# Optimization experiments

Hardware: AMD Instinct MI355X
Metric: run time of the kernel (lower is better)

## Reference

```python
import jax, jax.numpy as jnp
import numpy as np

B, H, W, C = 1, 64, 64, 256
HEADS, K, DIL = 8, 7, 2
HD = C // HEADS
FF = 4 * C
EPS = 1e-5
SCALE = 1.0 / float(np.sqrt(HD))


def _axis_indices(L, k, d):
    """NATTEN dilated neighborhood: per dilation-group clamped sliding window.
    Returns key indices [L,k] and relative-position-bias indices [L,k]."""
    i = np.arange(L)
    g, rem = i // d, i % d                      # position within dilation group
    lg = (L - rem + d - 1) // d                 # group length per position
    start = np.clip(g - k // 2, 0, lg - k)      # clamped window start (group coords)
    a = np.arange(k)
    kidx = (start[:, None] + a[None, :]) * d + rem[:, None]          # key coord
    bidx = start[:, None] + a[None, :] - g[:, None] + (k - 1)        # rpb coord in [0, 2k-2]
    return kidx.astype(np.int32), bidx.astype(np.int32)


def setup_inputs():
    key = jax.random.key(0)
    ks = jax.random.split(key, 8)
    p = lambda k_, sh: jax.random.normal(k_, sh, jnp.float32) * 0.02
    return {
        "x": jax.random.normal(ks[0], (B, H, W, C), jnp.float32),
        "ln1_g": jnp.ones((C,), jnp.float32), "ln1_b": jnp.zeros((C,), jnp.float32),
        "wq": p(ks[1], (C, C)), "bq": jnp.zeros((C,), jnp.float32),
        "wk": p(ks[2], (C, C)), "bk": jnp.zeros((C,), jnp.float32),
        "wv": p(ks[3], (C, C)), "bv": jnp.zeros((C,), jnp.float32),
        "rpb": p(ks[4], (HEADS, 2 * K - 1, 2 * K - 1)),
        "wo": p(ks[5], (C, C)), "bo": jnp.zeros((C,), jnp.float32),
        "ln2_g": jnp.ones((C,), jnp.float32), "ln2_b": jnp.zeros((C,), jnp.float32),
        "w1": p(ks[6], (C, FF)), "b1": jnp.zeros((FF,), jnp.float32),
        "w2": p(ks[7], (FF, C)), "b2": jnp.zeros((C,), jnp.float32),
    }


def _layer_norm(x, g, b):
    m = jnp.mean(x, -1, keepdims=True)
    v = jnp.mean(jnp.square(x - m), -1, keepdims=True)
    return (x - m) * jax.lax.rsqrt(v + EPS) * g + b


def reference(x, ln1_g, ln1_b, wq, bq, wk, bk, wv, bv, rpb, wo, bo,
              ln2_g, ln2_b, w1, b1, w2, b2):
    ih, bih = _axis_indices(H, K, DIL)   # [H,K]
    iw, biw = _axis_indices(W, K, DIL)   # [W,K]
    hs = _layer_norm(x, ln1_g, ln1_b)
    q = (hs @ wq + bq).reshape(B, H, W, HEADS, HD) * SCALE
    k = (hs @ wk + bk).reshape(B, H, W, HEADS, HD)
    v = (hs @ wv + bv).reshape(B, H, W, HEADS, HD)
    # gather dilated neighborhoods -> [B,H,W,K,K,heads,hd]
    k_nb = k[:, ih[:, None, :, None], iw[None, :, None, :], :, :]
    v_nb = v[:, ih[:, None, :, None], iw[None, :, None, :], :, :]
    # natten2dqkrpb: per-query scores over K*K dilated neighbors + rpb
    scores = jnp.einsum('bijnc,bijklnc->bnijkl', q, k_nb)
    bias = rpb[:, bih[:, None, :, None], biw[None, :, None, :]]  # [heads,H,W,K,K]
    scores = scores + bias[None]
    probs = jax.nn.softmax(scores.reshape(B, HEADS, H, W, K * K), axis=-1)
    # natten2dav
    ctx = jnp.einsum('bnijp,bijpnc->bijnc', probs,
                     v_nb.reshape(B, H, W, K * K, HEADS, HD))
    attn_out = ctx.reshape(B, H, W, C) @ wo + bo
    hs2 = x + attn_out                      # residual (layer_scale disabled: init 0.0)
    y = _layer_norm(hs2, ln2_g, ln2_b)
    y = jax.nn.gelu(y @ w1 + b1, approximate=False) @ w2 + b2
    return hs2 + y
```

## Files before the change

kernel.cpp:

```cpp
#include <hip/hip_runtime.h>
#include <math.h>

#define CC 256
#define NTOK 4096
#define NHEADS 8
#define HD 32
#define FFD 1024
#define LN_EPS 1e-5f
#define QSCALE 0.17677669529663687f

typedef __bf16 bf16x8 __attribute__((ext_vector_type(8)));
typedef float f32x4 __attribute__((ext_vector_type(4)));
typedef unsigned short u16x8 __attribute__((ext_vector_type(8)));

__device__ __forceinline__ unsigned short f2bf(float f) {
    unsigned u = __builtin_bit_cast(unsigned, f);
    u += 0x7fff + ((u >> 16) & 1);
    return (unsigned short)(u >> 16);
}
__device__ __forceinline__ float bf2f(unsigned short h) {
    unsigned u = ((unsigned)h) << 16;
    return __builtin_bit_cast(float, u);
}
__device__ __forceinline__ void gload16(const unsigned short* g, unsigned short* l) {
    __builtin_amdgcn_global_load_lds(
        (const __attribute__((address_space(1))) unsigned int*)(const void*)g,
        (__attribute__((address_space(3))) unsigned int*)(void*)l, 16, 0, 0);
}

__global__ void ln_kernel(const float* __restrict__ x, const float* __restrict__ g,
                          const float* __restrict__ b, unsigned short* __restrict__ out) {
    int wave = threadIdx.x >> 6;
    int lane = threadIdx.x & 63;
    int tok = blockIdx.x * 4 + wave;
    const float4 v = ((const float4*)(x + (size_t)tok * CC))[lane];
    float s  = v.x + v.y + v.z + v.w;
    float ss = v.x * v.x + v.y * v.y + v.z * v.z + v.w * v.w;
    #pragma unroll
    for (int o = 32; o > 0; o >>= 1) { s += __shfl_xor(s, o); ss += __shfl_xor(ss, o); }
    float m   = s * (1.0f / CC);
    float var = ss * (1.0f / CC) - m * m;
    float r   = rsqrtf(var + LN_EPS);
    float4 gv = ((const float4*)g)[lane];
    float4 bv = ((const float4*)b)[lane];
    ushort4 o4;
    o4.x = f2bf((v.x - m) * r * gv.x + bv.x);
    o4.y = f2bf((v.y - m) * r * gv.y + bv.y);
    o4.z = f2bf((v.z - m) * r * gv.z + bv.z);
    o4.w = f2bf((v.w - m) * r * gv.w + bv.w);
    ((ushort4*)(out + (size_t)tok * CC))[lane] = o4;
}

__global__ void setup_kernel(const float* __restrict__ wq, const float* __restrict__ wk,
                             const float* __restrict__ wv, const float* __restrict__ wo,
                             const float* __restrict__ w1, const float* __restrict__ w2,
                             const float* __restrict__ bq, const float* __restrict__ bk,
                             const float* __restrict__ bv,
                             unsigned short* __restrict__ wt_qkv, unsigned short* __restrict__ wo_t,
                             unsigned short* __restrict__ w1_t, unsigned short* __restrict__ w2_t,
                             float* __restrict__ bqkv) {
    int id = blockIdx.x;
    int t = threadIdx.x;
    if (id == 192) {
        bqkv[t]       = bq[t] * QSCALE;
        bqkv[256 + t] = bk[t];
        bqkv[512 + t] = bv[t];
        return;
    }
    const float* src; unsigned short* dst;
    int Kd, N, rowoff = 0, bx, by; float scale = 1.0f;
    if (id < 16)       { src = wq; dst = wt_qkv; Kd = 256;  N = 256;  scale = QSCALE; int l = id;       bx = l & 3;  by = l >> 2; }
    else if (id < 32)  { src = wk; dst = wt_qkv; Kd = 256;  N = 256;  rowoff = 256;   int l = id - 16;  bx = l & 3;  by = l >> 2; }
    else if (id < 48)  { src = wv; dst = wt_qkv; Kd = 256;  N = 256;  rowoff = 512;   int l = id - 32;  bx = l & 3;  by = l >> 2; }
    else if (id < 64)  { src = wo; dst = wo_t;   Kd = 256;  N = 256;                  int l = id - 48;  bx = l & 3;  by = l >> 2; }
    else if (id < 128) { src = w1; dst = w1_t;   Kd = 256;  N = 1024;                 int l = id - 64;  bx = l & 15; by = l >> 4; }
    else               { src = w2; dst = w2_t;   Kd = 1024; N = 256;                  int l = id - 128; bx = l & 3;  by = l >> 2; }
    int n0 = bx * 64, k0 = by * 64;
    __shared__ float tile[64][65];
    int cc = t & 63, rb = t >> 6;
    #pragma unroll
    for (int i = 0; i < 16; i++) {
        int r = rb + i * 4;
        tile[r][cc] = src[(size_t)(k0 + r) * N + n0 + cc];
    }
    __syncthreads();
    int n = t >> 2;
    #pragma unroll
    for (int i = 0; i < 8; i++) {
        int p = (t & 3) + i * 4;
        unsigned lo = f2bf(tile[2 * p][n] * scale);
        unsigned hi = f2bf(tile[2 * p + 1][n] * scale);
        *(unsigned*)(dst + (size_t)(rowoff + n0 + n) * Kd + k0 + 2 * p) = lo | (hi << 16);
    }
}

template<int BM, int BN, int KD, int ACT, bool ADD_RES, bool OUT_BF16>
__global__ __launch_bounds__(256) void gemm_db(
    const unsigned short* __restrict__ A, const unsigned short* __restrict__ Bt,
    const float* __restrict__ bias, const float* __restrict__ res,
    void* __restrict__ Cm, int N) {
    constexpr int WM = BM / 2, WN = BN / 2;
    constexpr int MF = WM / 16, NF = WN / 16;
    constexpr int NIT = KD / 64;
    __shared__ unsigned short lds[2][(BM + BN) * 64];
    const int t = threadIdx.x;
    const int lane = t & 63, w = t >> 6;
    const int wr = w >> 1, wc = w & 1;
    const int bm = blockIdx.y * BM, bn = blockIdx.x * BN;
    const int fr = lane & 15, sq = lane >> 4;

    auto stage = [&](int it, int buf) {
        unsigned short* La = lds[buf];
        unsigned short* Lb = lds[buf] + BM * 64;
        #pragma unroll
        for (int i = 0; i < BM * 8 / 256; i++) {
            int c = t + i * 256;
            int kk = c / (BM * 4), r = (c % (BM * 4)) >> 2, jj = c & 3;
            gload16(A + (size_t)(bm + r) * KD + it * 64 + kk * 32 + jj * 8, La + c * 8);
        }
        #pragma unroll
        for (int i = 0; i < BN * 8 / 256; i++) {
            int c = t + i * 256;
            int kk = c / (BN * 4), r = (c % (BN * 4)) >> 2, jj = c & 3;
            gload16(Bt + (size_t)(bn + r) * KD + it * 64 + kk * 32 + jj * 8, Lb + c * 8);
        }
    };

    f32x4 acc[MF][NF] = {};
    stage(0, 0);
    for (int it = 0; it < NIT; ++it) {
        const int buf = it & 1;
        __syncthreads();
        if (it + 1 < NIT) stage(it + 1, buf ^ 1);
        #pragma unroll
        for (int kk = 0; kk < 2; kk++) {
            const char* La = (const char*)(lds[buf]) + kk * BM * 64;
            const char* Lb = (const char*)(lds[buf] + BM * 64) + kk * BN * 64;
            bf16x8 af[MF], bfr[NF];
            #pragma unroll
            for (int i = 0; i < MF; i++)
                af[i] = *(const bf16x8*)(La + (wr * WM + i * 16 + fr) * 64 + sq * 16);
            #pragma unroll
            for (int j = 0; j < NF; j++)
                bfr[j] = *(const bf16x8*)(Lb + (wc * WN + j * 16 + fr) * 64 + sq * 16);
            #pragma unroll
            for (int i = 0; i < MF; i++)
                #pragma unroll
                for (int j = 0; j < NF; j++)
                    acc[i][j] = __builtin_amdgcn_mfma_f32_16x16x32_bf16(af[i], bfr[j], acc[i][j], 0, 0, 0);
        }
    }
    #pragma unroll
    for (int i = 0; i < MF; i++) {
        int row0 = bm + wr * WM + i * 16 + sq * 4;
        #pragma unroll
        for (int j = 0; j < NF; j++) {
            int col = bn + wc * WN + j * 16 + fr;
            float bvv = bias[col];
            #pragma unroll
            for (int r = 0; r < 4; r++) {
                float v = acc[i][j][r] + bvv;
                if constexpr (ACT == 1) v = 0.5f * v * (1.0f + erff(v * 0.70710678118654752f));
                if constexpr (ADD_RES) v += res[(size_t)(row0 + r) * N + col];
                if constexpr (OUT_BF16)
                    ((unsigned short*)Cm)[(size_t)(row0 + r) * N + col] = f2bf(v);
                else
                    ((float*)Cm)[(size_t)(row0 + r) * N + col] = v;
            }
        }
    }
}

__global__ __launch_bounds__(256) void attn_mfma(
    const unsigned short* __restrict__ qkv, const float* __restrict__ rpb,
    unsigned short* __restrict__ ctx) {
    __shared__ __align__(16) unsigned short VT[128][136];
    __shared__ __align__(16) unsigned short Pl[4][16][136];
    __shared__ unsigned short tbl[16][112];
    __shared__ float rpbl[4][172];

    const int t = threadIdx.x;
    const int lane = t & 63, w = t >> 6;
    const int fr = lane & 15, sq = lane >> 4;
    const int bid = blockIdx.x;
    const int p = bid & 3, tile = (bid >> 2) & 63, hb = bid >> 8;
    const int ri = p >> 1, rj = p & 1;
    const int tgi = (tile >> 3) * 4, tgj = (tile & 7) * 4;
    const int kgi0 = min(max(tgi - 3, 0), 22);
    const int kgj0 = min(max(tgj - 3, 0), 22);
    const int head = hb * 4 + w;

    for (int i = lane; i < 169; i += 64)
        rpbl[w][i] = rpb[head * 169 + i];
    if (lane == 0) rpbl[w][169] = -1e30f;

    for (int e = t; e < 16 * 112; e += 256) {
        int q = e / 112, kk = e % 112;
        unsigned short idx = 169;
        if (kk < 100) {
            int kr = kk / 10, kc = kk % 10;
            int qgi = tgi + (q >> 2), qgj = tgj + (q & 3);
            int kgi = kgi0 + kr, kgj = kgj0 + kc;
            int si = min(max(qgi - 3, 0), 25), sj = min(max(qgj - 3, 0), 25);
            if (kgi >= si && kgi <= si + 6 && kgj >= sj && kgj <= sj + 6)
                idx = (unsigned short)((kgi - qgi + 6) * 13 + (kgj - qgj + 6));
        }
        tbl[q][kk] = idx;
    }

    for (int c0 = t; c0 < 1600; c0 += 256) {
        int key = c0 >> 4, ch8 = c0 & 15;
        int kr = key / 10, kc = key % 10;
        int kt = ((kgi0 + kr) * 2 + ri) * 64 + (kgj0 + kc) * 2 + rj;
        u16x8 vv = *(const u16x8*)(qkv + (size_t)kt * 768 + 512 + hb * 128 + ch8 * 8);
        #pragma unroll
        for (int e = 0; e < 8; e++) VT[ch8 * 8 + e][key] = vv[e];
    }
    for (int c0 = t; c0 < 128 * 14; c0 += 256) {
        int row = c0 / 14, cp = c0 % 14;
        *(unsigned*)&VT[row][100 + cp * 2] = 0;
    }
    __syncthreads();

    const int qtok = ((tgi + (fr >> 2)) * 2 + ri) * 64 + (tgj + (fr & 3)) * 2 + rj;
    bf16x8 qf = *(const bf16x8*)(qkv + (size_t)qtok * 768 + head * 32 + sq * 8);

    f32x4 sc[7];
    #pragma unroll
    for (int c = 0; c < 7; c++) {
        int kk = c * 16 + fr;
        if (kk > 99) kk = 99;
        int kr = kk / 10, kc = kk % 10;
        int kt = ((kgi0 + kr) * 2 + ri) * 64 + (kgj0 + kc) * 2 + rj;
        bf16x8 kf = *(const bf16x8*)(qkv + (size_t)kt * 768 + 256 + head * 32 + sq * 8);
        f32x4 z = {0.0f, 0.0f, 0.0f, 0.0f};
        sc[c] = __builtin_amdgcn_mfma_f32_16x16x32_bf16(kf, qf, z, 0, 0, 0);
    }
    #pragma unroll
    for (int c = 0; c < 7; c++)
        #pragma unroll
        for (int r = 0; r < 4; r++) {
            int idx = tbl[fr][c * 16 + 4 * sq + r];
            sc[c][r] += rpbl[w][idx];
        }

    float mx = -1e30f;
    #pragma unroll
    for (int c = 0; c < 7; c++)
        #pragma unroll
        for (int r = 0; r < 4; r++) mx = fmaxf(mx, sc[c][r]);
    mx = fmaxf(mx, __shfl_xor(mx, 16));
    mx = fmaxf(mx, __shfl_xor(mx, 32));
    float sum = 0.0f;
    #pragma unroll
    for (int c = 0; c < 7; c++)
        #pragma unroll
        for (int r = 0; r < 4; r++) {
            sc[c][r] = __expf(sc[c][r] - mx);
            sum += sc[c][r];
        }
    sum += __shfl_xor(sum, 16);
    sum += __shfl_xor(sum, 32);
    float inv = 1.0f / sum;

    #pragma unroll
    for (int c = 0; c < 7; c++)
        #pragma unroll
        for (int r = 0; r < 4; r++)
            Pl[w][fr][c * 16 + 4 * sq + r] = f2bf(sc[c][r] * inv);
    *(unsigned long long*)&Pl[w][fr][112 + sq * 4] = 0ull;

    f32x4 o0 = {0, 0, 0, 0}, o1 = {0, 0, 0, 0};
    #pragma unroll
    for (int m = 0; m < 4; m++) {
        bf16x8 pf = *(const bf16x8*)(&Pl[w][fr][m * 32 + sq * 8]);
        bf16x8 v0 = *(const bf16x8*)(&VT[w * 32 + fr][m * 32 + sq * 8]);
        bf16x8 v1 = *(const bf16x8*)(&VT[w * 32 + 16 + fr][m * 32 + sq * 8]);
        o0 = __builtin_amdgcn_mfma_f32_16x16x32_bf16(pf, v0, o0, 0, 0, 0);
        o1 = __builtin_amdgcn_mfma_f32_16x16x32_bf16(pf, v1, o1, 0, 0, 0);
    }
    #pragma unroll
    for (int r = 0; r < 4; r++) {
        int tok = ((tgi + sq) * 2 + ri) * 64 + (tgj + r) * 2 + rj;
        ctx[(size_t)tok * 256 + head * 32 + fr]      = f2bf(o0[r]);
        ctx[(size_t)tok * 256 + head * 32 + 16 + fr] = f2bf(o1[r]);
    }
}

extern "C" void kernel_launch(void* const* d_in, const int* in_sizes, int n_in,
                              void* d_out, int out_size, void* d_ws, size_t ws_size,
                              hipStream_t stream) {
    const float* x     = (const float*)d_in[0];
    const float* ln1_g = (const float*)d_in[1];
    const float* ln1_b = (const float*)d_in[2];
    const float* wq    = (const float*)d_in[3];
    const float* bq    = (const float*)d_in[4];
    const float* wk    = (const float*)d_in[5];
    const float* bk    = (const float*)d_in[6];
    const float* wv    = (const float*)d_in[7];
    const float* bv    = (const float*)d_in[8];
    const float* rpb   = (const float*)d_in[9];
    const float* wo    = (const float*)d_in[10];
    const float* bo    = (const float*)d_in[11];
    const float* ln2_g = (const float*)d_in[12];
    const float* ln2_b = (const float*)d_in[13];
    const float* w1    = (const float*)d_in[14];
    const float* b1    = (const float*)d_in[15];
    const float* w2    = (const float*)d_in[16];
    const float* b2    = (const float*)d_in[17];

    char* wsb = (char*)d_ws;
    unsigned short* hs_bf  = (unsigned short*)(wsb);
    unsigned short* qkv_bf = (unsigned short*)(wsb + (2u << 20));
    unsigned short* ctx_bf = (unsigned short*)(wsb + (8u << 20));
    float*          hs2    = (float*)(wsb + (10u << 20));
    unsigned short* y1_bf  = (unsigned short*)(wsb + (14u << 20));
    unsigned short* gm_bf  = (unsigned short*)(wsb + (16u << 20));
    unsigned short* wt_qkv = (unsigned short*)(wsb + (24u << 20));
    unsigned short* wo_t   = wt_qkv + 768 * 256;
    unsigned short* w1_t   = wo_t + 256 * 256;
    unsigned short* w2_t   = w1_t + 1024 * 256;
    float*          bqkv   = (float*)(w2_t + 256 * 1024);

    setup_kernel<<<193, 256, 0, stream>>>(wq, wk, wv, wo, w1, w2, bq, bk, bv,
                                          wt_qkv, wo_t, w1_t, w2_t, bqkv);
    ln_kernel<<<NTOK / 4, 256, 0, stream>>>(x, ln1_g, ln1_b, hs_bf);
    gemm_db<64, 64, 256, 0, false, true><<<dim3(12, 64), 256, 0, stream>>>(
        hs_bf, wt_qkv, bqkv, nullptr, qkv_bf, 768);
    attn_mfma<<<512, 256, 0, stream>>>(qkv_bf, rpb, ctx_bf);
    gemm_db<32, 64, 256, 0, true, false><<<dim3(4, 128), 256, 0, stream>>>(
        ctx_bf, wo_t, bo, x, hs2, 256);
    ln_kernel<<<NTOK / 4, 256, 0, stream>>>(hs2, ln2_g, ln2_b, y1_bf);
    gemm_db<64, 64, 256, 1, false, true><<<dim3(16, 64), 256, 0, stream>>>(
        y1_bf, w1_t, b1, nullptr, gm_bf, 1024);
    gemm_db<32, 64, 1024, 0, true, false><<<dim3(4, 128), 256, 0, stream>>>(
        gm_bf, w2_t, b2, hs2, (float*)d_out, 256);
}
```

Baseline: 136.6 us.

## Triple-buffer GEMM loads, fuse LN1 into setup kernel, raise MFMA priority

The GEMM moves from double to triple buffered LDS staging, prefetching two iterations ahead. It replaces the full __syncthreads with explicit vmcnt waits plus a barrier so global loads overlap more of the MFMA work. The first layer norm is folded into the weight-setup launch as extra blocks, removing one kernel launch. The attention kernel also raises wave priority around its MFMA sections. These changes cost more LDS per block, which may lower occupancy, and they rely on hand-counted outstanding-load numbers.

```diff
diff --git a/kernel.cpp b/kernel.cpp
--- a/kernel.cpp
+++ b/kernel.cpp
@@ -28,11 +28,9 @@
         (__attribute__((address_space(3))) unsigned int*)(void*)l, 16, 0, 0);
 }
 
-__global__ void ln_kernel(const float* __restrict__ x, const float* __restrict__ g,
-                          const float* __restrict__ b, unsigned short* __restrict__ out) {
-    int wave = threadIdx.x >> 6;
-    int lane = threadIdx.x & 63;
-    int tok = blockIdx.x * 4 + wave;
+__device__ __forceinline__ void ln_row(const float* __restrict__ x, const float* __restrict__ g,
+                                       const float* __restrict__ b, unsigned short* __restrict__ out,
+                                       int tok, int lane) {
     const float4 v = ((const float4*)(x + (size_t)tok * CC))[lane];
     float s  = v.x + v.y + v.z + v.w;
     float ss = v.x * v.x + v.y * v.y + v.z * v.z + v.w * v.w;
@@ -51,16 +49,27 @@
     ((ushort4*)(out + (size_t)tok * CC))[lane] = o4;
 }
 
+__global__ void ln_kernel(const float* __restrict__ x, const float* __restrict__ g,
+                          const float* __restrict__ b, unsigned short* __restrict__ out) {
+    ln_row(x, g, b, out, blockIdx.x * 4 + (threadIdx.x >> 6), threadIdx.x & 63);
+}
+
 __global__ void setup_kernel(const float* __restrict__ wq, const float* __restrict__ wk,
                              const float* __restrict__ wv, const float* __restrict__ wo,
                              const float* __restrict__ w1, const float* __restrict__ w2,
                              const float* __restrict__ bq, const float* __restrict__ bk,
                              const float* __restrict__ bv,
+                             const float* __restrict__ x, const float* __restrict__ ln1_g,
+                             const float* __restrict__ ln1_b,
                              unsigned short* __restrict__ wt_qkv, unsigned short* __restrict__ wo_t,
                              unsigned short* __restrict__ w1_t, unsigned short* __restrict__ w2_t,
-                             float* __restrict__ bqkv) {
+                             float* __restrict__ bqkv, unsigned short* __restrict__ hs_bf) {
     int id = blockIdx.x;
     int t = threadIdx.x;
+    if (id >= 193) {
+        ln_row(x, ln1_g, ln1_b, hs_bf, (id - 193) * 4 + (t >> 6), t & 63);
+        return;
+    }
     if (id == 192) {
         bqkv[t]       = bq[t] * QSCALE;
         bqkv[256 + t] = bk[t];
@@ -95,14 +104,17 @@
 }
 
 template<int BM, int BN, int KD, int ACT, bool ADD_RES, bool OUT_BF16>
-__global__ __launch_bounds__(256) void gemm_db(
+__global__ __launch_bounds__(256) void gemm_tb(
     const unsigned short* __restrict__ A, const unsigned short* __restrict__ Bt,
     const float* __restrict__ bias, const float* __restrict__ res,
     void* __restrict__ Cm, int N) {
     constexpr int WM = BM / 2, WN = BN / 2;
     constexpr int MF = WM / 16, NF = WN / 16;
     constexpr int NIT = KD / 64;
-    __shared__ unsigned short lds[2][(BM + BN) * 64];
+    constexpr int LA = BM * 8 / 256;
+    constexpr int LB = BN * 8 / 256;
+    constexpr int L  = LA + LB;
+    __shared__ unsigned short lds[3][(BM + BN) * 64];
     const int t = threadIdx.x;
     const int lane = t & 63, w = t >> 6;
     const int wr = w >> 1, wc = w & 1;
@@ -113,13 +125,13 @@
         unsigned short* La = lds[buf];
         unsigned short* Lb = lds[buf] + BM * 64;
         #pragma unroll
-        for (int i = 0; i < BM * 8 / 256; i++) {
+        for (int i = 0; i < LA; i++) {
             int c = t + i * 256;
             int kk = c / (BM * 4), r = (c % (BM * 4)) >> 2, jj = c & 3;
             gload16(A + (size_t)(bm + r) * KD + it * 64 + kk * 32 + jj * 8, La + c * 8);
         }
         #pragma unroll
-        for (int i = 0; i < BN * 8 / 256; i++) {
+        for (int i = 0; i < LB; i++) {
             int c = t + i * 256;
             int kk = c / (BN * 4), r = (c % (BN * 4)) >> 2, jj = c & 3;
             gload16(Bt + (size_t)(bn + r) * KD + it * 64 + kk * 32 + jj * 8, Lb + c * 8);
@@ -128,10 +140,19 @@
 
     f32x4 acc[MF][NF] = {};
     stage(0, 0);
+    stage(1, 1);
+    #pragma unroll
     for (int it = 0; it < NIT; ++it) {
-        const int buf = it & 1;
-        __syncthreads();
-        if (it + 1 < NIT) stage(it + 1, buf ^ 1);
+        if (it < NIT - 1) {
+            if constexpr (L == 4) asm volatile("s_waitcnt vmcnt(4)" ::: "memory");
+            else if constexpr (L == 3) asm volatile("s_waitcnt vmcnt(3)" ::: "memory");
+            else asm volatile("s_waitcnt vmcnt(2)" ::: "memory");
+        } else {
+            asm volatile("s_waitcnt vmcnt(0)" ::: "memory");
+        }
+        __builtin_amdgcn_s_barrier();
+        if (it + 2 < NIT) stage(it + 2, (it + 2) % 3);
+        const int buf = it % 3;
         #pragma unroll
         for (int kk = 0; kk < 2; kk++) {
             const char* La = (const char*)(lds[buf]) + kk * BM * 64;
@@ -226,6 +247,7 @@
     bf16x8 qf = *(const bf16x8*)(qkv + (size_t)qtok * 768 + head * 32 + sq * 8);
 
     f32x4 sc[7];
+    __builtin_amdgcn_s_setprio(1);
     #pragma unroll
     for (int c = 0; c < 7; c++) {
         int kk = c * 16 + fr;
@@ -236,6 +258,7 @@
         f32x4 z = {0.0f, 0.0f, 0.0f, 0.0f};
         sc[c] = __builtin_amdgcn_mfma_f32_16x16x32_bf16(kf, qf, z, 0, 0, 0);
     }
+    __builtin_amdgcn_s_setprio(0);
     #pragma unroll
     for (int c = 0; c < 7; c++)
         #pragma unroll
@@ -271,6 +294,7 @@
     *(unsigned long long*)&Pl[w][fr][112 + sq * 4] = 0ull;
 
     f32x4 o0 = {0, 0, 0, 0}, o1 = {0, 0, 0, 0};
+    __builtin_amdgcn_s_setprio(1);
     #pragma unroll
     for (int m = 0; m < 4; m++) {
         bf16x8 pf = *(const bf16x8*)(&Pl[w][fr][m * 32 + sq * 8]);
@@ -279,6 +303,7 @@
         o0 = __builtin_amdgcn_mfma_f32_16x16x32_bf16(pf, v0, o0, 0, 0, 0);
         o1 = __builtin_amdgcn_mfma_f32_16x16x32_bf16(pf, v1, o1, 0, 0, 0);
     }
+    __builtin_amdgcn_s_setprio(0);
     #pragma unroll
     for (int r = 0; r < 4; r++) {
         int tok = ((tgi + sq) * 2 + ri) * 64 + (tgj + r) * 2 + rj;
@@ -322,17 +347,17 @@
     unsigned short* w2_t   = w1_t + 1024 * 256;
     float*          bqkv   = (float*)(w2_t + 256 * 1024);
 
-    setup_kernel<<<193, 256, 0, stream>>>(wq, wk, wv, wo, w1, w2, bq, bk, bv,
-                                          wt_qkv, wo_t, w1_t, w2_t, bqkv);
-    ln_kernel<<<NTOK / 4, 256, 0, stream>>>(x, ln1_g, ln1_b, hs_bf);
-    gemm_db<64, 64, 256, 0, false, true><<<dim3(12, 64), 256, 0, stream>>>(
+    setup_kernel<<<1217, 256, 0, stream>>>(wq, wk, wv, wo, w1, w2, bq, bk, bv,
+                                           x, ln1_g, ln1_b,
+                                           wt_qkv, wo_t, w1_t, w2_t, bqkv, hs_bf);
+    gemm_tb<64, 64, 256, 0, false, true><<<dim3(12, 64), 256, 0, stream>>>(
         hs_bf, wt_qkv, bqkv, nullptr, qkv_bf, 768);
     attn_mfma<<<512, 256, 0, stream>>>(qkv_bf, rpb, ctx_bf);
-    gemm_db<32, 64, 256, 0, true, false><<<dim3(4, 128), 256, 0, stream>>>(
+    gemm_tb<32, 64, 256, 0, true, false><<<dim3(4, 128), 256, 0, stream>>>(
         ctx_bf, wo_t, bo, x, hs2, 256);
     ln_kernel<<<NTOK / 4, 256, 0, stream>>>(hs2, ln2_g, ln2_b, y1_bf);
-    gemm_db<64, 64, 256, 1, false, true><<<dim3(16, 64), 256, 0, stream>>>(
+    gemm_tb<64, 64, 256, 1, false, true><<<dim3(16, 64), 256, 0, stream>>>(
         y1_bf, w1_t, b1, nullptr, gm_bf, 1024);
-    gemm_db<32, 64, 1024, 0, true, false><<<dim3(4, 128), 256, 0, stream>>>(
+    gemm_tb<32, 64, 1024, 0, true, false><<<dim3(4, 128), 256, 0, stream>>>(
         gm_bf, w2_t, b2, hs2, (float*)d_out, 256);
 }
```

Result: faster. 133.8 us (-2.0%).
